# Optimization experiments

Measured on AMD Instinct MI355X. Metric: run time of the kernel, lower is better.

Reference implementation:

```python
import jax, jax.numpy as jnp
import numpy as np

N = 512       # nodes
V = 8         # n_vectors_hidden
F = 128       # n_invariant_feat_hidden
H = 8         # num_heads
BESSEL = 8
R_MAX = 10.0
FH = F // H
VH = V // H

def _edges(n):
    s, r = np.meshgrid(np.arange(n), np.arange(n), indexing='ij')
    m = s != r
    return jnp.asarray(s[m], jnp.int32), jnp.asarray(r[m], jnp.int32)

def _sph(v):
    # real spherical harmonics ell=1,2,3, e3nn 'component' normalization, unit input v[...,3] -> [...,15]
    x, y, z = v[..., 0], v[..., 1], v[..., 2]
    s3, s15, s5 = np.sqrt(3.0), np.sqrt(15.0), np.sqrt(5.0)
    sh1 = jnp.stack([x, y, z], -1) * s3
    sh2 = jnp.stack([s15 * x * y, s15 * y * z, 0.5 * s5 * (3 * z**2 - 1), s15 * x * z, 0.5 * s15 * (x**2 - y**2)], -1)
    c33, c32, c31, c30 = np.sqrt(35.0 / 8.0), np.sqrt(105.0), np.sqrt(21.0 / 8.0), 0.5 * np.sqrt(7.0)
    sh3 = jnp.stack([c33 * y * (3 * x**2 - y**2), c32 * x * y * z, c31 * y * (5 * z**2 - 1), c30 * z * (5 * z**2 - 3), c31 * x * (5 * z**2 - 1), 0.5 * c32 * z * (x**2 - y**2), c33 * x * (x**2 - 3 * y**2)], -1)
    return jnp.concatenate([sh1, sh2, sh3], -1)

def _bessel(x, n, x_max):
    # e3nn.bessel basis: sqrt(2/x_max) * sin(k*pi*x/x_max) / x, k=1..n
    x = x[..., None]
    k = jnp.arange(1, n + 1, dtype=x.dtype)
    x_safe = jnp.where(x == 0, 1.0, x)
    return np.sqrt(2.0 / x_max) * jnp.sin(k * jnp.pi * x / x_max) / x_safe

def _sus(x):
    return jnp.where(x > 0, jnp.exp(-1.0 / jnp.where(x > 0, x, 1.0)), 0.0)

def _soft_envelope(x, x_max, a=2.0, v0=1.2):
    return v0 * _sus(a * (1.0 - x / x_max)) / _sus(jnp.asarray(a, x.dtype))

def _forward(positions, features, We0, be0, We1, be1, Wq, Wk, Wek, Wv, Wev, Wg, Wo0, bo0, Wo1, bo1, Wo2, bo2):
    n = positions.shape[0]
    senders, receivers = _edges(n)
    vec = positions[senders] - positions[receivers]               # [E,V,3] gather
    lengths = jnp.sqrt(jnp.sum(vec * vec, -1) + 1e-20)            # safe_norm [E,V]
    unit = vec / lengths[..., None]
    sph = _sph(unit)                                              # [E,V,15]
    radial = _bessel(lengths, BESSEL, R_MAX) * _soft_envelope(lengths, R_MAX)[..., None]  # [E,V,B]
    e_scal = radial.reshape(radial.shape[0], -1)                  # [E, V*B]
    h = jax.nn.silu(e_scal @ We0 + be0)
    h = jax.nn.silu(h @ We1 + be1)                                # edge MLP, output_activation=silu
    E = h.shape[0]
    q = (features @ Wq).reshape(n, H, FH)
    k = (features[senders] @ Wk + h @ Wek).reshape(E, H, FH)
    logits = jnp.einsum('ehf,ehf->eh', q[receivers], k) / np.sqrt(FH)
    seg_max = jax.ops.segment_max(logits, receivers, num_segments=n)
    ex = jnp.exp(logits - seg_max[receivers])                     # edge_weight_cutoff = 1
    denom = jax.ops.segment_sum(ex, receivers, num_segments=n)
    alpha = ex / denom[receivers]                                 # [E,H] per-receiver softmax
    v_s = (features[senders] @ Wv + h @ Wev).reshape(E, H, FH)
    gate = h @ Wg                                                 # [E,V] invariant gates
    v_vec = (gate[..., None] * sph[..., :3]).reshape(E, H, VH, 3) # equivariant values from ell=1 sph
    agg_s = jax.ops.segment_sum(alpha[..., None] * v_s, receivers, num_segments=n).reshape(n, F)
    agg_v = jax.ops.segment_sum(alpha[:, :, None, None] * v_vec, receivers, num_segments=n).reshape(n, V, 3)
    o = jax.nn.silu(agg_s @ Wo0 + bo0)
    o = jax.nn.silu(o @ Wo1 + bo1)
    o = o @ Wo2 + bo2                                             # hk MLP: last layer linear
    return (positions + agg_v, features + o)

def setup_inputs() -> dict:
    key = jax.random.key(0)
    ks = jax.random.split(key, 16)
    def w(k, i, o):
        return jax.random.normal(k, (i, o), jnp.float32) / np.sqrt(i)
    M = 128
    D = V * BESSEL
    return {
        'positions': jax.random.normal(ks[0], (N, V, 3), jnp.float32),
        'features': jax.random.normal(ks[1], (N, F), jnp.float32),
        'We0': w(ks[2], D, M), 'be0': jnp.zeros((M,), jnp.float32),
        'We1': w(ks[3], M, M), 'be1': jnp.zeros((M,), jnp.float32),
        'Wq': w(ks[4], F, F), 'Wk': w(ks[5], F, F), 'Wek': w(ks[6], M, F),
        'Wv': w(ks[7], F, F), 'Wev': w(ks[8], M, F), 'Wg': w(ks[9], M, V),
        'Wo0': w(ks[10], F, M), 'bo0': jnp.zeros((M,), jnp.float32),
        'Wo1': w(ks[11], M, M), 'bo1': jnp.zeros((M,), jnp.float32),
        'Wo2': w(ks[12], M, F), 'bo2': jnp.zeros((F,), jnp.float32),
    }

def reference(positions, features, We0, be0, We1, be1, Wq, Wk, Wek, Wv, Wev, Wg, Wo0, bo0, Wo1, bo1, Wo2, bo2):
    return _forward(positions, features, We0, be0, We1, be1, Wq, Wk, Wek, Wv, Wev, Wg, Wo0, bo0, Wo1, bo1, Wo2, bo2)
```

## Files before the change

### kernel.cpp

```cpp
#include <hip/hip_runtime.h>
#include <hip/hip_bf16.h>

#define WS_KNB  0
#define WS_VNT  32768
#define WS_AW2  65536
#define WS_W0T  1114112
#define WS_W1T  1118208
#define WS_PS   1126400
#define PS_STRIDE 1072

typedef short bf16x8 __attribute__((ext_vector_type(8)));
typedef short short4v __attribute__((ext_vector_type(4)));
typedef float f32x4 __attribute__((ext_vector_type(4)));
typedef unsigned short ushort_t;

static __device__ __forceinline__ ushort_t f2b(float x) {
  __hip_bfloat16 h = __float2bfloat16(x);
  return reinterpret_cast<ushort_t&>(h);
}
static __device__ __forceinline__ float b2f(ushort_t u) {
  unsigned v = ((unsigned)u) << 16;
  return reinterpret_cast<float&>(v);
}
static __device__ __forceinline__ float fsilu(float x) {
  return x * __builtin_amdgcn_rcpf(1.f + __expf(-x));
}

static __device__ __forceinline__ bf16x8 radial_frag(
    float dx, float dy, float dz, float& ux, float& uy, float& uz)
{
  const float l2 = fmaf(dx,dx, fmaf(dy,dy, fmaf(dz,dz, 1e-20f)));
  const float inv = rsqrtf(l2);
  const float len = l2 * inv;
  ux = dx*inv; uy = dy*inv; uz = dz*inv;
  const float yy = 2.f - len*0.2f;
  const float env = (yy > 0.f) ? 1.9784655648f * __expf(-__builtin_amdgcn_rcpf(yy)) : 0.f;
  const float coef = 0.4472135955f * env * inv;
  const float arg = len * 0.31415926535f;
  const float s1v = __sinf(arg), c1v = __cosf(arg);
  const float twc = 2.f*c1v;
  float sp = 0.f, sc = s1v;
  bf16x8 ev;
#pragma unroll
  for (int bb = 0; bb < 8; ++bb) {
    ev[bb] = (short)f2b(coef*sc);
    const float nx = fmaf(twc, sc, -sp);
    sp = sc; sc = nx;
  }
  return ev;
}

__global__ __launch_bounds__(128) void k_prep(
    const float* __restrict__ feat, const float* __restrict__ Wq,
    const float* __restrict__ Wk, const float* __restrict__ Wv,
    const float* __restrict__ Wek, const float* __restrict__ Wg,
    const float* __restrict__ We0, const float* __restrict__ We1,
    float* __restrict__ ws)
{
  const int blk = blockIdx.x, j = threadIdx.x;
  if (blk >= 512) {
    const int i = (blk - 512)*128 + j;
    ushort_t* W0T = (ushort_t*)(ws + WS_W0T);
    ushort_t* W1T = (ushort_t*)(ws + WS_W1T);
    if (i < 8192) {
      const int n = i >> 6, k = i & 63;
      W0T[n*64 + k] = f2b(We0[k*128 + n]);
    } else {
      const int t = i - 8192, n = t >> 7, k = t & 127;
      W1T[n*128 + k] = f2b(We1[k*128 + n]);
    }
    return;
  }
  const int r = blk;
  __shared__ float fr[128];
  __shared__ float qL[128];
  fr[j] = feat[r*128 + j];
  __syncthreads();
  float aq = 0.f, ak = 0.f, av = 0.f;
#pragma unroll 4
  for (int i = 0; i < 128; ++i) {
    const float f = fr[i];
    aq = fmaf(f, Wq[i*128 + j], aq);
    ak = fmaf(f, Wk[i*128 + j], ak);
    av = fmaf(f, Wv[i*128 + j], av);
  }
  ushort_t* knB = (ushort_t*)(ws + WS_KNB);
  ushort_t* vnT = (ushort_t*)(ws + WS_VNT);
  knB[r*128 + j] = f2b(ak);
  vnT[j*512 + r] = f2b(av);
  qL[j] = aq;
  __syncthreads();
  ushort_t* AW = (ushort_t*)(ws + WS_AW2) + r*4096;
  const float* wr = Wek + j*128;
  const int jh = j >> 4;
#pragma unroll
  for (int h = 0; h < 8; ++h) {
    float acc = 0.f;
#pragma unroll
    for (int f = 0; f < 16; ++f)
      acc = fmaf(wr[16*h + f], qL[16*h + f], acc);
    AW[h*256 + j] = f2b(acc * 0.25f);
    AW[h*256 + 128 + j] = (h == jh) ? f2b(0.25f * aq) : (ushort_t)0;
  }
#pragma unroll
  for (int v = 0; v < 8; ++v) {
    AW[(8 + v)*256 + j] = f2b(Wg[j*8 + v]);
    AW[(8 + v)*256 + 128 + j] = 0;
  }
}

#define MFMA(a,b,c) __builtin_amdgcn_mfma_f32_16x16x32_bf16((a),(b),(c),0,0,0)

__global__ __launch_bounds__(512, 4) void k_edge13(
    const float* __restrict__ pos,
    const float* __restrict__ be0, const float* __restrict__ be1,
    float* __restrict__ ws)
{
  __shared__ __align__(16) char Lds[40960];
  ushort_t* H1   = (ushort_t*)(Lds);
  ushort_t* Pb   = (ushort_t*)(Lds);
  float*    rscL = (float*)(Lds + 2048);
  ushort_t* H2t  = (ushort_t*)(Lds + 16384);
  ushort_t* Es   = (ushort_t*)(Lds + 32768);
  float*    lgT0 = (float*)(Lds + 32768);
  float*    lgT1 = (float*)(Lds + 36864);

  const int tid = threadIdx.x;
  const int nw = tid >> 6, l = tid & 63;
  const int c = l & 15, g = l >> 4;
  const int b = blockIdx.x;
  const int r = b >> 1, half = b & 1;
  const int base = half * 256;

  const ushort_t* knB = (const ushort_t*)(ws + WS_KNB);
  const ushort_t* vnT = (const ushort_t*)(ws + WS_VNT);
  const ushort_t* AW2 = (const ushort_t*)(ws + WS_AW2) + r*4096;
  const ushort_t* W0T = (const ushort_t*)(ws + WS_W0T);
  const ushort_t* W1T = (const ushort_t*)(ws + WS_W1T);

  const int ncol = nw*16 + c;
  const float be0v = be0[ncol], be1v = be1[ncol];
  const int m_lg = nw & 3, kh = nw >> 2;
  const int ncswz = ((ncol & 7) ^ ((ncol >> 3) & 7)) & 7;

  const float prx = pos[r*24 + nw*3 + 0];
  const float pry = pos[r*24 + nw*3 + 1];
  const float prz = pos[r*24 + nw*3 + 2];

  f32x4 bh = {0,0,0,0}, sna = {0,0,0,0};
  float avx = 0.f, avy = 0.f, avz = 0.f;
  float mrun = -1e30f, drun = 0.f;
  float ux, uy, uz;

  {
    const int sg = base + l;
    const bf16x8 ev = radial_frag(pos[sg*24 + nw*3 + 0] - prx,
                                  pos[sg*24 + nw*3 + 1] - pry,
                                  pos[sg*24 + nw*3 + 2] - prz, ux, uy, uz);
    *(bf16x8*)(Es + l*64 + ((nw ^ (l&7))<<3)) = ev;
  }
  __syncthreads();

  for (int tile = 0; tile < 4; ++tile) {
    const int gbase = base + tile*64;

    float npx = 0.f, npy = 0.f, npz = 0.f;
    if (tile < 3) {
      const int sg = gbase + 64 + l;
      npx = pos[sg*24 + nw*3 + 0];
      npy = pos[sg*24 + nw*3 + 1];
      npz = pos[sg*24 + nw*3 + 2];
    }

    {
      const bf16x8 w0f0 = *(const bf16x8*)(W0T + ncol*64 + g*8);
      const bf16x8 w0f1 = *(const bf16x8*)(W0T + ncol*64 + 32 + g*8);
#pragma unroll
      for (int m = 0; m < 4; ++m) {
        const int ra = m*16 + c;
        const bf16x8 e0 = *(const bf16x8*)(Es + ra*64 + (((g  ) ^ (ra&7))<<3));
        const bf16x8 e1 = *(const bf16x8*)(Es + ra*64 + (((4+g) ^ (ra&7))<<3));
        f32x4 acc = {0,0,0,0};
        acc = MFMA(e0, w0f0, acc);
        acc = MFMA(e1, w0f1, acc);
#pragma unroll
        for (int i = 0; i < 4; ++i) {
          const int row = m*16 + g*4 + i;
          H1[row*128 + (((ncol>>3) ^ (row&15))<<3) + (c&7)] =
              f2b(fsilu(acc[i] + be0v));
        }
      }
    }
    __syncthreads();

#pragma unroll
    for (int m = 0; m < 4; ++m) {
      const int ra = m*16 + c;
      f32x4 acc = {0,0,0,0};
#pragma unroll
      for (int kb = 0; kb < 4; ++kb) {
        const bf16x8 af = *(const bf16x8*)(H1 + ra*128 + (((kb*4+g) ^ (ra&15))<<3));
        const bf16x8 wf = *(const bf16x8*)(W1T + ncol*128 + kb*32 + g*8);
        acc = MFMA(af, wf, acc);
      }
      short4v pk;
#pragma unroll
      for (int i = 0; i < 4; ++i)
        pk[i] = (short)f2b(fsilu(acc[i] + be1v));
      *(short4v*)(H2t + ncol*64 +
          ((((m*2 + (g>>1)) ^ ncswz) & 7)<<3) + (g&1)*4) = pk;
    }
    __syncthreads();

    {
      f32x4 lg = {0,0,0,0};
      if (kh == 0) {
        const int rb = m_lg*2 + (c>>3);
        const int rl = c & 7;
#pragma unroll
        for (int kb = 0; kb < 4; ++kb) {
          const int cc = (kb*4 + g) & 7;
          bf16x8 bb;
#pragma unroll
          for (int j = 0; j < 8; ++j)
            bb[j] = (short)H2t[(kb*32 + g*8 + j)*64 +
                               (((rb ^ j ^ cc) & 7)<<3) + rl];
          const bf16x8 aw = *(const bf16x8*)(AW2 + c*256 + kb*32 + g*8);
          lg = MFMA(aw, bb, lg);
        }
      } else {
        const int srow = gbase + m_lg*16 + c;
#pragma unroll
        for (int kb = 0; kb < 4; ++kb) {
          const bf16x8 bb = *(const bf16x8*)(knB + srow*128 + kb*32 + g*8);
          const bf16x8 aw = *(const bf16x8*)(AW2 + c*256 + 128 + kb*32 + g*8);
          lg = MFMA(aw, bb, lg);
        }
      }
      float* lgW = kh ? lgT1 : lgT0;
#pragma unroll
      for (int i = 0; i < 4; ++i) {
        const int ch = g*4 + i;
        lgW[ch*64 + ((m_lg*16 + c) ^ (g<<4))] = lg[i];
      }
    }
    __syncthreads();

    {
      const int h = nw;
      const int kv = (h>>2)<<4;
      const int kg = ((8+h)>>2)<<4;
      float lgv = lgT0[h*64 + (l ^ kv)] + lgT1[h*64 + (l ^ kv)];
      const float gate = lgT0[(8+h)*64 + (l ^ kg)] + lgT1[(8+h)*64 + (l ^ kg)];
      if (gbase + l == r) lgv = -1e30f;
      float t = lgv;
      t = fmaxf(t, __shfl_xor(t, 1));
      t = fmaxf(t, __shfl_xor(t, 2));
      t = fmaxf(t, __shfl_xor(t, 4));
      t = fmaxf(t, __shfl_xor(t, 8));
      t = fmaxf(t, __shfl_xor(t, 16));
      t = fmaxf(t, __shfl_xor(t, 32));
      const float mnew = fmaxf(mrun, t);
      const float rsc = __expf(mrun - mnew);
      mrun = mnew;
      const float val = __expf(lgv - mnew);
      float wsm = val;
      wsm += __shfl_xor(wsm, 1);
      wsm += __shfl_xor(wsm, 2);
      wsm += __shfl_xor(wsm, 4);
      wsm += __shfl_xor(wsm, 8);
      wsm += __shfl_xor(wsm, 16);
      wsm += __shfl_xor(wsm, 32);
      drun = drun*rsc + wsm;
      const float ga = val * gate;
      Pb[h*64 + (((l>>3) ^ h)<<3) + (l&7)] = f2b(val);
      Pb[(8+h)*64 + (((l>>3) ^ h)<<3) + (l&7)] = f2b(ga);
      if (l == 0) rscL[h] = rsc;
      avx = avx*rsc + ga*ux;
      avy = avy*rsc + ga*uy;
      avz = avz*rsc + ga*uz;
    }
    __syncthreads();

    {
      float rs[4];
#pragma unroll
      for (int i = 0; i < 4; ++i) rs[i] = rscL[(4*g + i) & 7];
#pragma unroll
      for (int i = 0; i < 4; ++i) { bh[i] *= rs[i]; sna[i] *= rs[i]; }
      const bf16x8 pa0 = *(const bf16x8*)(Pb + c*64 + (((g  ) ^ (c&7))<<3));
      const bf16x8 pa1 = *(const bf16x8*)(Pb + c*64 + (((4+g) ^ (c&7))<<3));
      bh = MFMA(pa0, *(const bf16x8*)(H2t + ncol*64 +
               ((((g  ) ^ ncswz) & 7)<<3)), bh);
      bh = MFMA(pa1, *(const bf16x8*)(H2t + ncol*64 +
               ((((4+g) ^ ncswz) & 7)<<3)), bh);
      const bf16x8 vnf0 = *(const bf16x8*)(vnT + ncol*512 + gbase + g*8);
      const bf16x8 vnf1 = *(const bf16x8*)(vnT + ncol*512 + gbase + 32 + g*8);
      sna = MFMA(pa0, vnf0, sna);
      sna = MFMA(pa1, vnf1, sna);
    }
    if (tile < 3) {
      const bf16x8 ev = radial_frag(npx - prx, npy - pry, npz - prz, ux, uy, uz);
      *(bf16x8*)(Es + l*64 + ((nw ^ (l&7))<<3)) = ev;
      __syncthreads();
    }
  }

  float* PSf = ws + WS_PS + b*PS_STRIDE;
  ushort_t* PSs = (ushort_t*)PSf;
  if (g < 2) {
#pragma unroll
    for (int i = 0; i < 4; ++i) {
      PSs[(4*g + i)*128 + ncol] = f2b(bh[i]);
      PSs[1024 + (4*g + i)*128 + ncol] = f2b(sna[i]);
    }
  }
  avx += __shfl_xor(avx, 1); avy += __shfl_xor(avy, 1); avz += __shfl_xor(avz, 1);
  avx += __shfl_xor(avx, 2); avy += __shfl_xor(avy, 2); avz += __shfl_xor(avz, 2);
  avx += __shfl_xor(avx, 4); avy += __shfl_xor(avy, 4); avz += __shfl_xor(avz, 4);
  avx += __shfl_xor(avx, 8); avy += __shfl_xor(avy, 8); avz += __shfl_xor(avz, 8);
  avx += __shfl_xor(avx,16); avy += __shfl_xor(avy,16); avz += __shfl_xor(avz,16);
  avx += __shfl_xor(avx,32); avy += __shfl_xor(avy,32); avz += __shfl_xor(avz,32);
  if (l == 0) {
    PSf[1024 + nw*3 + 0] = avx;
    PSf[1024 + nw*3 + 1] = avy;
    PSf[1024 + nw*3 + 2] = avz;
    PSf[1048 + nw] = mrun;
    PSf[1056 + nw] = drun;
  }
}

__global__ __launch_bounds__(128) void k_merge(
    const float* __restrict__ pos, const float* __restrict__ feat,
    const float* __restrict__ Wev,
    const float* __restrict__ Wo0, const float* __restrict__ bo0,
    const float* __restrict__ Wo1, const float* __restrict__ bo1,
    const float* __restrict__ Wo2, const float* __restrict__ bo2,
    const float* __restrict__ ws, float* __restrict__ out)
{
  const int r = blockIdx.x, j = threadIdx.x;
  __shared__ float S1s[8], S2s[8], Dh[8];
  __shared__ float BhC[1024];
  __shared__ float asB[128], o1[128], o2[128];
  const float* P1f = ws + WS_PS + (2*r)*PS_STRIDE;
  const float* P2f = P1f + PS_STRIDE;
  const ushort_t* P1s = (const ushort_t*)P1f;
  const ushort_t* P2s = (const ushort_t*)P2f;
  if (j < 8) {
    const float m1 = P1f[1048 + j], m2 = P2f[1048 + j];
    const float M = fmaxf(m1, m2);
    const float s1 = __expf(m1 - M), s2 = __expf(m2 - M);
    S1s[j] = s1; S2s[j] = s2;
    Dh[j] = s1*P1f[1056 + j] + s2*P2f[1056 + j];
  }
  __syncthreads();
#pragma unroll
  for (int h = 0; h < 8; ++h)
    BhC[h*128 + j] = S1s[h]*b2f(P1s[h*128 + j]) + S2s[h]*b2f(P2s[h*128 + j]);
  const int hh = j >> 4;
  const float snj = S1s[hh]*b2f(P1s[1024 + hh*128 + j])
                  + S2s[hh]*b2f(P2s[1024 + hh*128 + j]);
  if (j < 24) {
    const int v = j / 3;
    const float avc = S1s[v]*P1f[1024 + j] + S2s[v]*P2f[1024 + j];
    out[r*24 + j] = pos[r*24 + j]
        + 1.7320508076f * avc * __builtin_amdgcn_rcpf(Dh[v]);
  }
  __syncthreads();
  {
    float ev = 0.f;
#pragma unroll 4
    for (int m = 0; m < 128; ++m)
      ev = fmaf(BhC[hh*128 + m], Wev[m*128 + j], ev);
    asB[j] = (snj + ev) * __builtin_amdgcn_rcpf(Dh[hh]);
  }
  __syncthreads();
  {
    float acc = bo0[j];
#pragma unroll 4
    for (int i = 0; i < 128; ++i) acc = fmaf(asB[i], Wo0[i*128 + j], acc);
    o1[j] = fsilu(acc);
  }
  __syncthreads();
  {
    float acc = bo1[j];
#pragma unroll 4
    for (int i = 0; i < 128; ++i) acc = fmaf(o1[i], Wo1[i*128 + j], acc);
    o2[j] = fsilu(acc);
  }
  __syncthreads();
  {
    float acc = bo2[j];
#pragma unroll 4
    for (int i = 0; i < 128; ++i) acc = fmaf(o2[i], Wo2[i*128 + j], acc);
    out[12288 + r*128 + j] = feat[r*128 + j] + acc;
  }
}

extern "C" void kernel_launch(void* const* d_in, const int* in_sizes, int n_in,
                              void* d_out, int out_size, void* d_ws, size_t ws_size,
                              hipStream_t stream)
{
  const float* pos  = (const float*)d_in[0];
  const float* feat = (const float*)d_in[1];
  const float* We0  = (const float*)d_in[2];
  const float* be0  = (const float*)d_in[3];
  const float* We1  = (const float*)d_in[4];
  const float* be1  = (const float*)d_in[5];
  const float* Wq   = (const float*)d_in[6];
  const float* Wk   = (const float*)d_in[7];
  const float* Wek  = (const float*)d_in[8];
  const float* Wv   = (const float*)d_in[9];
  const float* Wev  = (const float*)d_in[10];
  const float* Wg   = (const float*)d_in[11];
  const float* Wo0  = (const float*)d_in[12];
  const float* bo0  = (const float*)d_in[13];
  const float* Wo1  = (const float*)d_in[14];
  const float* bo1  = (const float*)d_in[15];
  const float* Wo2  = (const float*)d_in[16];
  const float* bo2  = (const float*)d_in[17];
  float* ws  = (float*)d_ws;
  float* out = (float*)d_out;

  hipLaunchKernelGGL(k_prep, dim3(704), dim3(128), 0, stream,
                     feat, Wq, Wk, Wv, Wek, Wg, We0, We1, ws);
  hipLaunchKernelGGL(k_edge13, dim3(1024), dim3(512), 0, stream,
                     pos, be0, be1, ws);
  hipLaunchKernelGGL(k_merge, dim3(512), dim3(128), 0, stream,
                     pos, feat, Wev, Wo0, bo0, Wo1, bo1, Wo2, bo2, ws, out);
}
```

Measured before the change: 104.2 us.

## Split each receiver's senders across four blocks and compact per-receiver attention weights

The edge kernel now gives each receiver four blocks of 128 senders each, where before it used two blocks of 256, doubling the grid to 2048 blocks. The merge kernel now combines four partial softmax states instead of two. The prep kernel no longer writes a padded 4096-entry per-receiver weight matrix. Instead it stores a compact 1024-entry A4 block per receiver, a shared transposed Wg, and the scaled query vector, and the edge kernel builds the block-diagonal query operand in registers. The aim is more parallelism to fill the GPU and less workspace traffic, at the cost of more partial-state writes and extra merge work.

Result: faster. 101.7 us (-2.4%).

```diff
diff --git a/kernel.cpp b/kernel.cpp
--- a/kernel.cpp
+++ b/kernel.cpp
@@ -3,10 +3,12 @@
 
 #define WS_KNB  0
 #define WS_VNT  32768
-#define WS_AW2  65536
-#define WS_W0T  1114112
-#define WS_W1T  1118208
-#define WS_PS   1126400
+#define WS_QNB  65536
+#define WS_A4T  98304
+#define WS_WGT  360448
+#define WS_W0T  360960
+#define WS_W1T  365056
+#define WS_PS   373248
 #define PS_STRIDE 1072
 
 typedef short bf16x8 __attribute__((ext_vector_type(8)));
@@ -86,32 +88,33 @@
   }
   ushort_t* knB = (ushort_t*)(ws + WS_KNB);
   ushort_t* vnT = (ushort_t*)(ws + WS_VNT);
+  ushort_t* qnB = (ushort_t*)(ws + WS_QNB);
   knB[r*128 + j] = f2b(ak);
   vnT[j*512 + r] = f2b(av);
+  qnB[r*128 + j] = f2b(0.25f * aq);
   qL[j] = aq;
   __syncthreads();
-  ushort_t* AW = (ushort_t*)(ws + WS_AW2) + r*4096;
+  ushort_t* A4 = (ushort_t*)(ws + WS_A4T) + r*1024;
   const float* wr = Wek + j*128;
-  const int jh = j >> 4;
 #pragma unroll
   for (int h = 0; h < 8; ++h) {
     float acc = 0.f;
 #pragma unroll
     for (int f = 0; f < 16; ++f)
       acc = fmaf(wr[16*h + f], qL[16*h + f], acc);
-    AW[h*256 + j] = f2b(acc * 0.25f);
-    AW[h*256 + 128 + j] = (h == jh) ? f2b(0.25f * aq) : (ushort_t)0;
-  }
-#pragma unroll
-  for (int v = 0; v < 8; ++v) {
-    AW[(8 + v)*256 + j] = f2b(Wg[j*8 + v]);
-    AW[(8 + v)*256 + 128 + j] = 0;
+    A4[h*128 + j] = f2b(acc * 0.25f);
+  }
+  if (r == 0) {
+    ushort_t* WgT = (ushort_t*)(ws + WS_WGT);
+#pragma unroll
+    for (int v = 0; v < 8; ++v)
+      WgT[v*128 + j] = f2b(Wg[j*8 + v]);
   }
 }
 
 #define MFMA(a,b,c) __builtin_amdgcn_mfma_f32_16x16x32_bf16((a),(b),(c),0,0,0)
 
-__global__ __launch_bounds__(512, 4) void k_edge13(
+__global__ __launch_bounds__(512, 4) void k_edge14(
     const float* __restrict__ pos,
     const float* __restrict__ be0, const float* __restrict__ be1,
     float* __restrict__ ws)
@@ -129,12 +132,14 @@
   const int nw = tid >> 6, l = tid & 63;
   const int c = l & 15, g = l >> 4;
   const int b = blockIdx.x;
-  const int r = b >> 1, half = b & 1;
-  const int base = half * 256;
+  const int r = b >> 2, quarter = b & 3;
+  const int base = quarter * 128;
 
   const ushort_t* knB = (const ushort_t*)(ws + WS_KNB);
   const ushort_t* vnT = (const ushort_t*)(ws + WS_VNT);
-  const ushort_t* AW2 = (const ushort_t*)(ws + WS_AW2) + r*4096;
+  const ushort_t* qnB = (const ushort_t*)(ws + WS_QNB);
+  const ushort_t* A4G = (const ushort_t*)(ws + WS_A4T) + r*1024;
+  const ushort_t* WgG = (const ushort_t*)(ws + WS_WGT);
   const ushort_t* W0T = (const ushort_t*)(ws + WS_W0T);
   const ushort_t* W1T = (const ushort_t*)(ws + WS_W1T);
 
@@ -161,11 +166,11 @@
   }
   __syncthreads();
 
-  for (int tile = 0; tile < 4; ++tile) {
+  for (int tile = 0; tile < 2; ++tile) {
     const int gbase = base + tile*64;
 
     float npx = 0.f, npy = 0.f, npz = 0.f;
-    if (tile < 3) {
+    if (tile < 1) {
       const int sg = gbase + 64 + l;
       npx = pos[sg*24 + nw*3 + 0];
       npy = pos[sg*24 + nw*3 + 1];
@@ -217,6 +222,7 @@
       if (kh == 0) {
         const int rb = m_lg*2 + (c>>3);
         const int rl = c & 7;
+        const ushort_t* ab = (c < 8) ? (A4G + c*128) : (WgG + (c-8)*128);
 #pragma unroll
         for (int kb = 0; kb < 4; ++kb) {
           const int cc = (kb*4 + g) & 7;
@@ -225,7 +231,7 @@
           for (int j = 0; j < 8; ++j)
             bb[j] = (short)H2t[(kb*32 + g*8 + j)*64 +
                                (((rb ^ j ^ cc) & 7)<<3) + rl];
-          const bf16x8 aw = *(const bf16x8*)(AW2 + c*256 + kb*32 + g*8);
+          const bf16x8 aw = *(const bf16x8*)(ab + kb*32 + g*8);
           lg = MFMA(aw, bb, lg);
         }
       } else {
@@ -233,7 +239,11 @@
 #pragma unroll
         for (int kb = 0; kb < 4; ++kb) {
           const bf16x8 bb = *(const bf16x8*)(knB + srow*128 + kb*32 + g*8);
-          const bf16x8 aw = *(const bf16x8*)(AW2 + c*256 + 128 + kb*32 + g*8);
+          const bf16x8 qf = *(const bf16x8*)(qnB + r*128 + kb*32 + g*8);
+          bf16x8 aw;
+          const bool hit = (kb*2 + (g>>1)) == c;
+#pragma unroll
+          for (int j = 0; j < 8; ++j) aw[j] = hit ? qf[j] : (short)0;
           lg = MFMA(aw, bb, lg);
         }
       }
@@ -299,7 +309,7 @@
       sna = MFMA(pa0, vnf0, sna);
       sna = MFMA(pa1, vnf1, sna);
     }
-    if (tile < 3) {
+    if (tile < 1) {
       const bf16x8 ev = radial_frag(npx - prx, npy - pry, npz - prz, ux, uy, uz);
       *(bf16x8*)(Es + l*64 + ((nw ^ (l&7))<<3)) = ev;
       __syncthreads();
@@ -339,30 +349,49 @@
     const float* __restrict__ ws, float* __restrict__ out)
 {
   const int r = blockIdx.x, j = threadIdx.x;
-  __shared__ float S1s[8], S2s[8], Dh[8];
+  __shared__ float Ss[32], Dh[8];
   __shared__ float BhC[1024];
   __shared__ float asB[128], o1[128], o2[128];
-  const float* P1f = ws + WS_PS + (2*r)*PS_STRIDE;
-  const float* P2f = P1f + PS_STRIDE;
-  const ushort_t* P1s = (const ushort_t*)P1f;
-  const ushort_t* P2s = (const ushort_t*)P2f;
+  const float* Pf[4];
+  const ushort_t* Ps[4];
+#pragma unroll
+  for (int i = 0; i < 4; ++i) {
+    Pf[i] = ws + WS_PS + (4*r + i)*PS_STRIDE;
+    Ps[i] = (const ushort_t*)Pf[i];
+  }
   if (j < 8) {
-    const float m1 = P1f[1048 + j], m2 = P2f[1048 + j];
-    const float M = fmaxf(m1, m2);
-    const float s1 = __expf(m1 - M), s2 = __expf(m2 - M);
-    S1s[j] = s1; S2s[j] = s2;
-    Dh[j] = s1*P1f[1056 + j] + s2*P2f[1056 + j];
-  }
-  __syncthreads();
-#pragma unroll
-  for (int h = 0; h < 8; ++h)
-    BhC[h*128 + j] = S1s[h]*b2f(P1s[h*128 + j]) + S2s[h]*b2f(P2s[h*128 + j]);
+    float M = -1e30f;
+#pragma unroll
+    for (int i = 0; i < 4; ++i) M = fmaxf(M, Pf[i][1048 + j]);
+    float D = 0.f;
+#pragma unroll
+    for (int i = 0; i < 4; ++i) {
+      const float s = __expf(Pf[i][1048 + j] - M);
+      Ss[i*8 + j] = s;
+      D = fmaf(s, Pf[i][1056 + j], D);
+    }
+    Dh[j] = D;
+  }
+  __syncthreads();
+#pragma unroll
+  for (int h = 0; h < 8; ++h) {
+    float acc = 0.f;
+#pragma unroll
+    for (int i = 0; i < 4; ++i)
+      acc = fmaf(Ss[i*8 + h], b2f(Ps[i][h*128 + j]), acc);
+    BhC[h*128 + j] = acc;
+  }
   const int hh = j >> 4;
-  const float snj = S1s[hh]*b2f(P1s[1024 + hh*128 + j])
-                  + S2s[hh]*b2f(P2s[1024 + hh*128 + j]);
+  float snj = 0.f;
+#pragma unroll
+  for (int i = 0; i < 4; ++i)
+    snj = fmaf(Ss[i*8 + hh], b2f(Ps[i][1024 + hh*128 + j]), snj);
   if (j < 24) {
     const int v = j / 3;
-    const float avc = S1s[v]*P1f[1024 + j] + S2s[v]*P2f[1024 + j];
+    float avc = 0.f;
+#pragma unroll
+    for (int i = 0; i < 4; ++i)
+      avc = fmaf(Ss[i*8 + v], Pf[i][1024 + j], avc);
     out[r*24 + j] = pos[r*24 + j]
         + 1.7320508076f * avc * __builtin_amdgcn_rcpf(Dh[v]);
   }
@@ -424,7 +453,7 @@
 
   hipLaunchKernelGGL(k_prep, dim3(704), dim3(128), 0, stream,
                      feat, Wq, Wk, Wv, Wek, Wg, We0, We1, ws);
-  hipLaunchKernelGGL(k_edge13, dim3(1024), dim3(512), 0, stream,
+  hipLaunchKernelGGL(k_edge14, dim3(2048), dim3(512), 0, stream,
                      pos, be0, be1, ws);
   hipLaunchKernelGGL(k_merge, dim3(512), dim3(128), 0, stream,
                      pos, feat, Wev, Wo0, bo0, Wo1, bo1, Wo2, bo2, ws, out);
```
